# Performance work log

Hardware: AMD Instinct MI355X
Metric: run time of the kernel (lower is better)

Reference implementation:

```python
import jax, jax.numpy as jnp
import numpy as np

NQ = 7
DIM = 2 ** NQ  # 128
N_LAYERS = 3

# Pauli-Z sign tables over the 128 basis states (wire 0 = most significant bit)
_bits = ((np.arange(DIM)[None, :] >> (NQ - 1 - np.arange(NQ)[:, None])) & 1)
_SZ = (1.0 - 2.0 * _bits).astype(np.float32)            # [7, 128]
_SZZ = (_SZ * np.roll(_SZ, -1, axis=0)).astype(np.float32)  # [7, 128], Z_i Z_{(i+1)%7}


def _cnot_perm(c, t):
    # CNOT is a basis-state permutation: flip target bit where control bit = 1
    k = np.arange(DIM)
    return k ^ (((k >> (NQ - 1 - c)) & 1) << (NQ - 1 - t))


def _apply_ry(state, theta, q):
    # state: [B, 128] complex64; theta: [B] or scalar (real)
    B = state.shape[0]
    s = state.reshape(B, 2 ** q, 2, 2 ** (NQ - 1 - q))
    c = jnp.reshape(jnp.cos(0.5 * theta), (-1, 1, 1))
    sn = jnp.reshape(jnp.sin(0.5 * theta), (-1, 1, 1))
    a0, a1 = s[:, :, 0, :], s[:, :, 1, :]
    return jnp.stack([c * a0 - sn * a1, sn * a0 + c * a1], axis=2).reshape(B, DIM)


def _apply_rz(state, theta, q):
    B = state.shape[0]
    s = state.reshape(B, 2 ** q, 2, 2 ** (NQ - 1 - q))
    p = jnp.reshape(jnp.exp(-0.5j * theta), (-1, 1, 1))  # diag(e^{-i t/2}, e^{+i t/2})
    return jnp.stack([p * s[:, :, 0, :], jnp.conj(p) * s[:, :, 1, :]], axis=2).reshape(B, DIM)


def _circuit(x_q, scales, biases, wry, wrz):
    # Batched 7-qubit state-vector simulation of quantum_circuit_v3
    B = x_q.shape[0]
    state = jnp.zeros((B, DIM), jnp.complex64).at[:, 0].set(1.0)
    ang = scales[None, :] * x_q + biases[None, :]  # [B, 7] encoding angles (same every layer)
    for layer in range(N_LAYERS):
        for i in range(NQ):
            state = _apply_ry(state, ang[:, i], i)
        for i in range(NQ):
            state = _apply_ry(state, wry[layer, i], i)
            state = _apply_rz(state, wrz[layer, i], i)
        shift = layer + 1
        for i in range(NQ):
            state = state[:, _cnot_perm(i, (i + shift) % NQ)]
    probs = state.real ** 2 + state.imag ** 2  # [B, 128]
    return jnp.concatenate([probs @ _SZ.T, probs @ _SZZ.T], axis=1)  # [B, 14]


def setup_inputs() -> dict:
    key = jax.random.key(0)
    ks = jax.random.split(key, 16)
    B, F = 32768, 64
    fus_in = 14 + 32 + F  # 110
    lin = lambda k, fi, fo: (0.05 * jax.random.normal(k, (fi, fo), jnp.float32))
    d = {
        "x_q": jax.random.uniform(ks[0], (B, NQ), jnp.float32),
        "x_c": jax.random.normal(ks[1], (B, F), jnp.float32),
        "input_scales": jnp.full((NQ,), np.pi, jnp.float32),
        "input_biases": jnp.zeros((NQ,), jnp.float32),
        "q_params_ry": 0.1 * jax.random.normal(ks[2], (N_LAYERS, NQ), jnp.float32),
        "q_params_rz": 0.1 * jax.random.normal(ks[3], (N_LAYERS, NQ), jnp.float32),
        "enc_w1": lin(ks[4], F, 64), "enc_b1": jnp.zeros((64,), jnp.float32),
        "enc_w2": lin(ks[5], 64, 32), "enc_b2": jnp.zeros((32,), jnp.float32),
        "fus_w1": lin(ks[6], fus_in, 128), "fus_b1": jnp.zeros((128,), jnp.float32),
        "fus_w2": lin(ks[7], 128, 64), "fus_b2": jnp.zeros((64,), jnp.float32),
        "fus_w3": lin(ks[8], 64, 32), "fus_b3": jnp.zeros((32,), jnp.float32),
        "fus_w4": lin(ks[9], 32, 1), "fus_b4": jnp.zeros((1,), jnp.float32),
    }
    return d


def reference(x_q, x_c, input_scales, input_biases, q_params_ry, q_params_rz,
              enc_w1, enc_b1, enc_w2, enc_b2,
              fus_w1, fus_b1, fus_w2, fus_b2, fus_w3, fus_b3, fus_w4, fus_b4):
    q_out = _circuit(x_q, input_scales, input_biases, q_params_ry, q_params_rz)  # [B, 14]
    h = jax.nn.relu(x_c @ enc_w1 + enc_b1)
    c_enc = jax.nn.relu(h @ enc_w2 + enc_b2)  # [B, 32]
    comb = jnp.concatenate([q_out, c_enc, x_c], axis=1)  # [B, 110]
    h = jax.nn.relu(comb @ fus_w1 + fus_b1)
    h = jax.nn.relu(h @ fus_w2 + fus_b2)
    h = jax.nn.relu(h @ fus_w3 + fus_b3)
    return (h @ fus_w4 + fus_b4)[:, 0]  # [B], dropout is identity at inference
```

## Files before the change

kernel.cpp:

```cpp
#include <hip/hip_runtime.h>
#include <math.h>

#define NQ 7
#define DIM 128
#define NLAYERS 3
#define ROWS 64
#define LDS_S 136

typedef __attribute__((ext_vector_type(8))) short bf16x8;
typedef __attribute__((ext_vector_type(4))) float f32x4;
typedef __attribute__((ext_vector_type(4))) unsigned short us4;

__device__ __forceinline__ unsigned short f2bf(float x) {
    union { float f; unsigned int u; } v; v.f = x;
    unsigned int r = v.u + 0x7fff + ((v.u >> 16) & 1);
    return (unsigned short)(r >> 16);
}

constexpr int cperm(int k, int c, int t) {
    return k ^ (((k >> (6 - c)) & 1) << (6 - t));
}
constexpr int lgather(int k, int s) {
    int r = k;
    for (int i = 6; i >= 0; --i) r = cperm(r, i, (i + s) % 7);
    return r;
}

struct Mat { int c[7]; };

constexpr Mat ID{{1, 2, 4, 8, 16, 32, 64}};

constexpr int parity7(int x) { x ^= x >> 4; x ^= x >> 2; x ^= x >> 1; return x & 1; }

constexpr int mapv(const Mat& A, int v) {
    int r = 0;
    for (int j = 0; j < 7; ++j) if ((v >> j) & 1) r ^= A.c[j];
    return r;
}
constexpr Mat matmul(const Mat& A, const Mat& B) {
    Mat m{};
    for (int j = 0; j < 7; ++j) m.c[j] = mapv(A, B.c[j]);
    return m;
}
constexpr Mat matG(int L) {
    Mat m{};
    for (int j = 0; j < 7; ++j) m.c[j] = lgather(1 << j, L + 1);
    return m;
}
constexpr Mat matinv(const Mat& A) {
    int M[7] = {};
    for (int r = 0; r < 7; ++r) {
        int row = 0;
        for (int j = 0; j < 7; ++j) row |= ((A.c[j] >> r) & 1) << j;
        M[r] = row | (1 << (7 + r));
    }
    for (int col = 0; col < 7; ++col) {
        int piv = col;
        while (!((M[piv] >> col) & 1)) ++piv;
        int t = M[col]; M[col] = M[piv]; M[piv] = t;
        for (int r = 0; r < 7; ++r)
            if (r != col && ((M[r] >> col) & 1)) M[r] ^= M[col];
    }
    Mat inv{};
    for (int j = 0; j < 7; ++j) {
        int c = 0;
        for (int r = 0; r < 7; ++r) c |= ((M[r] >> (7 + j)) & 1) << r;
        inv.c[j] = c;
    }
    return inv;
}
constexpr bool isident(const Mat& A) {
    for (int j = 0; j < 7; ++j) if (A.c[j] != (1 << j)) return false;
    return true;
}

constexpr Mat LAM1  = matinv(matG(0));
constexpr Mat LAM2  = matmul(matinv(matG(1)), LAM1);
constexpr Mat LAM3  = matmul(matinv(matG(2)), LAM2);
constexpr Mat LAM1I = matG(0);
constexpr Mat LAM2I = matinv(LAM2);
static_assert(isident(matmul(LAM1, LAM1I)), "lam1 inv");
static_assert(isident(matmul(LAM2, LAM2I)), "lam2 inv");
static_assert(isident(matmul(matG(2), matmul(LAM3, matinv(LAM2)))), "lam3 chain");

constexpr int rowmask(const Mat& A, int b) {
    int r = 0;
    for (int j = 0; j < 7; ++j) r |= ((A.c[j] >> b) & 1) << j;
    return r;
}
constexpr int featM(const Mat& A, int m) {
    int M = 0;
    for (int j = 0; j < 7; ++j) M |= parity7(A.c[j] & m) << j;
    return M;
}
constexpr int szzmask(int i) { return (1 << (6 - i)) | (1 << (6 - ((i + 1) % 7))); }

template<int M>
__device__ __forceinline__ float xsh(float v) {
    if constexpr (M == 1 || M == 2 || M == 3) {
        constexpr int ctrl = (0 ^ M) | ((1 ^ M) << 2) | ((2 ^ M) << 4) | ((3 ^ M) << 6);
        return __int_as_float(__builtin_amdgcn_update_dpp(
            __float_as_int(v), __float_as_int(v), ctrl, 0xF, 0xF, true));
    } else if constexpr (M == 7) {
        return __int_as_float(__builtin_amdgcn_update_dpp(
            __float_as_int(v), __float_as_int(v), 0x141, 0xF, 0xF, true));
    } else if constexpr (M == 15) {
        return __int_as_float(__builtin_amdgcn_update_dpp(
            __float_as_int(v), __float_as_int(v), 0x140, 0xF, 0xF, true));
    } else {
        return __shfl_xor(v, M, 64);
    }
}

template<int D, int R>
__device__ __forceinline__ void ryg(float c, float s, int lane,
                                    float& x0r, float& x0i, float& x1r, float& x1i)
{
    constexpr int  DL = D & 63;
    constexpr int  RL = R & 63;
    constexpr bool D6 = (D >> 6) & 1;
    constexpr bool R6 = (R >> 6) & 1;
    int par = __popc(lane & RL) & 1;
    float ns = -s;
    float sg0 = par ? s : ns;
    float sg1 = R6 ? (par ? ns : s) : sg0;
    float p0r, p0i, p1r, p1i;
    if constexpr (D6) {
        if constexpr (DL == 0) { p0r = x1r; p0i = x1i; p1r = x0r; p1i = x0i; }
        else {
            p0r = xsh<DL>(x1r); p0i = xsh<DL>(x1i);
            p1r = xsh<DL>(x0r); p1i = xsh<DL>(x0i);
        }
    } else {
        p0r = xsh<DL>(x0r); p0i = xsh<DL>(x0i);
        p1r = xsh<DL>(x1r); p1i = xsh<DL>(x1i);
    }
    x0r = fmaf(c, x0r, sg0 * p0r); x0i = fmaf(c, x0i, sg0 * p0i);
    x1r = fmaf(c, x1r, sg1 * p1r); x1i = fmaf(c, x1i, sg1 * p1i);
}

template<int LYR, int I>
__device__ __forceinline__ void rygates(
    const float* trig,
    const float (&dc)[2][NQ], const float (&dsn)[2][NQ], int lane,
    float (&A0r)[2], float (&A0i)[2], float (&A1r)[2], float (&A1i)[2])
{
    if constexpr (I < NQ) {
        constexpr Mat LM  = (LYR == 1) ? LAM1 : LAM2;
        constexpr Mat LMI = (LYR == 1) ? LAM1I : LAM2I;
        constexpr int b   = 6 - I;
        constexpr int D   = mapv(LMI, 1 << b);
        constexpr int R   = rowmask(LM, b);
        float cw = trig[(LYR * NQ + I) * 2 + 0];
        float sw = trig[(LYR * NQ + I) * 2 + 1];
#pragma unroll
        for (int e = 0; e < 2; ++e) {
            float c = dc[e][I] * cw - dsn[e][I] * sw;
            float s = dsn[e][I] * cw + dc[e][I] * sw;
            ryg<D, R>(c, s, lane, A0r[e], A0i[e], A1r[e], A1i[e]);
        }
        rygates<LYR, I + 1>(trig, dc, dsn, lane, A0r, A0i, A1r, A1i);
    }
}

template<int LYR, int Q>
__device__ __forceinline__ void rzrows(const float* __restrict__ wrz, int lane,
                                       float& Aacc, float& Bacc)
{
    if constexpr (Q < NQ) {
        constexpr Mat LM = (LYR == 0) ? ID : ((LYR == 1) ? LAM1 : LAM2);
        constexpr int R  = rowmask(LM, 6 - Q);
        float h = 0.5f * wrz[LYR * NQ + Q];
        float t = (__popc(lane & (R & 63)) & 1) ? -h : h;
        if constexpr ((R >> 6) & 1) Bacc += t; else Aacc += t;
        rzrows<LYR, Q + 1>(wrz, lane, Aacc, Bacc);
    }
}

template<int LYR>
__device__ __forceinline__ void rzlayer(const float* __restrict__ wrz, int lane,
    float (&A0r)[2], float (&A0i)[2], float (&A1r)[2], float (&A1i)[2])
{
    float Aacc = 0.0f, Bacc = 0.0f;
    rzrows<LYR, 0>(wrz, lane, Aacc, Bacc);
    float th0 = Aacc + Bacc, th1 = Aacc - Bacc;
    float c0 = __cosf(th0), s0 = __sinf(th0);
    float c1 = __cosf(th1), s1 = __sinf(th1);
#pragma unroll
    for (int e = 0; e < 2; ++e) {
        float r = A0r[e], im = A0i[e];
        A0r[e] = fmaf(c0, r, s0 * im);
        A0i[e] = fmaf(c0, im, -s0 * r);
        r = A1r[e]; im = A1i[e];
        A1r[e] = fmaf(c1, r, s1 * im);
        A1i[e] = fmaf(c1, im, -s1 * r);
    }
}

template<int M>
__device__ __forceinline__ void bfly(int lane, float& tp, float& tm) {
    float pp = xsh<M>(tp), pm = xsh<M>(tm);
    bool hi = (lane & M) != 0;
    tp = hi ? (pp - tp) : (tp + pp);
    tm = hi ? (pm - tm) : (tm + pm);
}

template<int F>
__device__ __forceinline__ void feats(int lane, float tp, float tm,
                                      float* __restrict__ qo) {
    if constexpr (F < 14) {
        constexpr int m = (F < 7) ? (64 >> F) : szzmask(F - 7);
        constexpr int M = featM(LAM3, m);
        if (lane == (M & 63)) qo[F] = ((M >> 6) & 1) ? tm : tp;
        feats<F + 1>(lane, tp, tm, qo);
    }
}

__global__ __launch_bounds__(256) void circuit_kernel(
    const float* __restrict__ x_q, const float* __restrict__ scales,
    const float* __restrict__ biases,
    const float* __restrict__ wry, const float* __restrict__ wrz,
    const float* __restrict__ ew1, const float* __restrict__ ew2,
    const float* __restrict__ w1,  const float* __restrict__ w2,
    const float* __restrict__ w3,  const float* __restrict__ w4,
    float* __restrict__ q_out,
    unsigned short* __restrict__ ew1t, unsigned short* __restrict__ ew2t,
    unsigned short* __restrict__ w1t,  unsigned short* __restrict__ w2t,
    unsigned short* __restrict__ w3t,  unsigned short* __restrict__ w4t,
    int B)
{
    __shared__ float strig[NLAYERS * NQ * 2];
    const int tid  = threadIdx.x;
    const int lane = tid & 63;

    if (tid < NLAYERS * NQ) {
        float hy = 0.5f * wry[tid];
        strig[tid * 2 + 0] = __cosf(hy);
        strig[tid * 2 + 1] = __sinf(hy);
    }

    if (blockIdx.x < 64) {
        const int gbase  = blockIdx.x * 256 + tid;
        const int stride = 64 * 256;
        for (int i = gbase; i < 16384; i += stride) {
            int n = i >> 7, kp = i & 127;
            unsigned short v = 0;
            if (kp < 64)        v = f2bf(w1[(46 + kp) * 128 + n]);
            else if (kp < 78)   v = f2bf(w1[(kp - 64) * 128 + n]);
            else if (kp < 110)  v = f2bf(w1[(kp - 78 + 14) * 128 + n]);
            w1t[i] = v;
        }
        for (int i = gbase; i < 8192; i += stride) {
            int n = i >> 7, k = i & 127;
            w2t[i] = f2bf(w2[k * 64 + n]);
        }
        for (int i = gbase; i < 4096; i += stride) {
            int n = i >> 6, k = i & 63;
            ew1t[i] = f2bf(ew1[k * 64 + n]);
        }
        for (int i = gbase; i < 2048; i += stride) {
            int n = i >> 6, k = i & 63;
            ew2t[i] = f2bf(ew2[k * 32 + n]);
        }
        for (int i = gbase; i < 2048; i += stride) {
            int n = i >> 6, k = i & 63;
            w3t[i] = f2bf(w3[k * 32 + n]);
        }
        for (int i = gbase; i < 512; i += stride) {
            int n = i >> 5, k = i & 31;
            w4t[i] = (n == 0) ? f2bf(w4[k]) : (unsigned short)0;
        }
    }
    __syncthreads();

    int gtid = blockIdx.x * blockDim.x + tid;
    int wv   = gtid >> 6;
    int e0   = wv * 2;
    if (e0 >= B) return;

    float dc[2][NQ], dsn[2][NQ];
#pragma unroll
    for (int e = 0; e < 2; ++e)
#pragma unroll
        for (int i = 0; i < NQ; ++i) {
            float h = 0.5f * fmaf(scales[i], x_q[(e0 + e) * NQ + i], biases[i]);
            dc[e][i]  = __cosf(h);
            dsn[e][i] = __sinf(h);
        }

    float A0r[2], A0i[2], A1r[2], A1i[2];
#pragma unroll
    for (int e = 0; e < 2; ++e) {
        float cl[NQ], sl[NQ];
#pragma unroll
        for (int i = 0; i < NQ; ++i) {
            float cw = strig[i * 2 + 0], sw = strig[i * 2 + 1];
            cl[i] = dc[e][i] * cw - dsn[e][i] * sw;
            sl[i] = dsn[e][i] * cw + dc[e][i] * sw;
        }
        float f1 = (lane & 32) ? sl[1] : cl[1];
        float f2 = (lane & 16) ? sl[2] : cl[2];
        float f3 = (lane &  8) ? sl[3] : cl[3];
        float f4 = (lane &  4) ? sl[4] : cl[4];
        float f5 = (lane &  2) ? sl[5] : cl[5];
        float f6 = (lane &  1) ? sl[6] : cl[6];
        float pr = (f1 * f2) * (f3 * f4) * (f5 * f6);
        A0r[e] = pr * cl[0]; A0i[e] = 0.0f;
        A1r[e] = pr * sl[0]; A1i[e] = 0.0f;
    }

    rzlayer<0>(wrz, lane, A0r, A0i, A1r, A1i);
    rygates<1, 0>(strig, dc, dsn, lane, A0r, A0i, A1r, A1i);
    rzlayer<1>(wrz, lane, A0r, A0i, A1r, A1i);
    rygates<2, 0>(strig, dc, dsn, lane, A0r, A0i, A1r, A1i);
    rzlayer<2>(wrz, lane, A0r, A0i, A1r, A1i);

#pragma unroll
    for (int e = 0; e < 2; ++e) {
        float p0 = A0r[e] * A0r[e] + A0i[e] * A0i[e];
        float p1 = A1r[e] * A1r[e] + A1i[e] * A1i[e];
        float tp = p0 + p1;
        float tm = p0 - p1;

        bfly<1>(lane, tp, tm);
        bfly<2>(lane, tp, tm);
        bfly<4>(lane, tp, tm);
        bfly<8>(lane, tp, tm);
        bfly<16>(lane, tp, tm);
        bfly<32>(lane, tp, tm);

        feats<0>(lane, tp, tm, q_out + (size_t)(e0 + e) * 14);
    }
}

template<int K, int NTILES, bool RELU>
__device__ __forceinline__ void layer_mfma(
    const unsigned short* src, unsigned short* dst,
    const unsigned short* __restrict__ wt, const float* __restrict__ bias,
    int dstcol, int lane, int wv)
{
    constexpr int KB   = K / 32;
    constexpr int NT_W = (NTILES > 4) ? NTILES / 4 : 1;
    constexpr int MT_W = NTILES / NT_W;
    const int ntile0 = (wv * NT_W) % NTILES;
    const int mtile0 = ((wv * NT_W) / NTILES) * MT_W;
    const int lcol = lane & 15;
    const int lrow = lane >> 4;

    bf16x8 bfrag[NT_W][KB];
    float  bb[NT_W];
#pragma unroll
    for (int n = 0; n < NT_W; ++n) {
#pragma unroll
        for (int kb = 0; kb < KB; ++kb)
            bfrag[n][kb] = *(const bf16x8*)&wt[((ntile0 + n) * 16 + lcol) * K + kb * 32 + lrow * 8];
        bb[n] = bias[(ntile0 + n) * 16 + lcol];
    }

#pragma unroll
    for (int m = 0; m < MT_W; ++m) {
        bf16x8 afrag[KB];
#pragma unroll
        for (int kb = 0; kb < KB; ++kb)
            afrag[kb] = *(const bf16x8*)&src[((mtile0 + m) * 16 + lcol) * LDS_S + kb * 32 + lrow * 8];

        f32x4 acc[NT_W];
#pragma unroll
        for (int n = 0; n < NT_W; ++n) acc[n] = (f32x4){bb[n], bb[n], bb[n], bb[n]};
#pragma unroll
        for (int kb = 0; kb < KB; ++kb)
#pragma unroll
            for (int n = 0; n < NT_W; ++n)
                acc[n] = __builtin_amdgcn_mfma_f32_16x16x32_bf16(afrag[kb], bfrag[n][kb], acc[n], 0, 0, 0);

#pragma unroll
        for (int n = 0; n < NT_W; ++n)
#pragma unroll
            for (int r = 0; r < 4; ++r) {
                float v = acc[n][r];
                if (RELU) v = fmaxf(v, 0.0f);
                dst[((mtile0 + m) * 16 + lrow * 4 + r) * LDS_S + dstcol + (ntile0 + n) * 16 + lcol] = f2bf(v);
            }
    }
}

__global__ __launch_bounds__(256, 4) void mlp_kernel(
    const float* __restrict__ q_out, const float* __restrict__ x_c,
    const unsigned short* __restrict__ ew1t, const float* __restrict__ eb1,
    const unsigned short* __restrict__ ew2t, const float* __restrict__ eb2,
    const unsigned short* __restrict__ w1t,  const float* __restrict__ b1,
    const unsigned short* __restrict__ w2t,  const float* __restrict__ b2,
    const unsigned short* __restrict__ w3t,  const float* __restrict__ b3,
    const unsigned short* __restrict__ w4t,  const float* __restrict__ b4,
    float* __restrict__ out, int B)
{
    __shared__ unsigned short BufA[ROWS * LDS_S];
    __shared__ unsigned short BufB[ROWS * LDS_S];

    const int tid  = threadIdx.x;
    const int lane = tid & 63;
    const int wv   = __builtin_amdgcn_readfirstlane(tid >> 6);
    const int base = blockIdx.x * ROWS;

    {
        const float4* xr = (const float4*)(x_c + (size_t)base * 64);
        for (int i = tid; i < 1024; i += 256) {
            int row = i >> 4, fc = i & 15;
            float4 v = xr[i];
            us4 b;
            b.x = f2bf(v.x); b.y = f2bf(v.y); b.z = f2bf(v.z); b.w = f2bf(v.w);
            *(us4*)&BufA[row * LDS_S + fc * 4] = b;
        }
    }
    for (int i = tid; i < 64 * 14; i += 256) {
        int row = i / 14, k = i - row * 14;
        BufA[row * LDS_S + 64 + k] = f2bf(q_out[(size_t)(base + row) * 14 + k]);
    }
    for (int i = tid; i < 64 * 18; i += 256) {
        int row = i / 18, k = i - row * 18;
        BufA[row * LDS_S + 110 + k] = 0;
    }
    __syncthreads();

    layer_mfma<64, 4, true>(BufA, BufB, ew1t, eb1, 0, lane, wv);
    __syncthreads();
    layer_mfma<64, 2, true>(BufB, BufA, ew2t, eb2, 78, lane, wv);
    __syncthreads();
    layer_mfma<128, 8, true>(BufA, BufB, w1t, b1, 0, lane, wv);
    __syncthreads();
    layer_mfma<128, 4, true>(BufB, BufA, w2t, b2, 0, lane, wv);
    __syncthreads();
    layer_mfma<64, 2, true>(BufA, BufB, w3t, b3, 0, lane, wv);
    __syncthreads();

    {
        const int lcol = lane & 15;
        const int lrow = lane >> 4;
        bf16x8 a = *(const bf16x8*)&BufB[(wv * 16 + lcol) * LDS_S + lrow * 8];
        bf16x8 b = *(const bf16x8*)&w4t[lcol * 32 + lrow * 8];
        float bv = b4[0];
        f32x4 acc = (f32x4){bv, bv, bv, bv};
        acc = __builtin_amdgcn_mfma_f32_16x16x32_bf16(a, b, acc, 0, 0, 0);
        if (lcol == 0) {
            float4 o; o.x = acc[0]; o.y = acc[1]; o.z = acc[2]; o.w = acc[3];
            *(float4*)(out + base + wv * 16 + lrow * 4) = o;
        }
    }
}

extern "C" void kernel_launch(void* const* d_in, const int* in_sizes, int n_in,
                              void* d_out, int out_size, void* d_ws, size_t ws_size,
                              hipStream_t stream)
{
    const float* x_q     = (const float*)d_in[0];
    const float* x_c     = (const float*)d_in[1];
    const float* scales  = (const float*)d_in[2];
    const float* biases  = (const float*)d_in[3];
    const float* wry     = (const float*)d_in[4];
    const float* wrz     = (const float*)d_in[5];
    const float* enc_w1  = (const float*)d_in[6];
    const float* enc_b1  = (const float*)d_in[7];
    const float* enc_w2  = (const float*)d_in[8];
    const float* enc_b2  = (const float*)d_in[9];
    const float* fus_w1  = (const float*)d_in[10];
    const float* fus_b1  = (const float*)d_in[11];
    const float* fus_w2  = (const float*)d_in[12];
    const float* fus_b2  = (const float*)d_in[13];
    const float* fus_w3  = (const float*)d_in[14];
    const float* fus_b3  = (const float*)d_in[15];
    const float* fus_w4  = (const float*)d_in[16];
    const float* fus_b4  = (const float*)d_in[17];
    float* out = (float*)d_out;

    int B = in_sizes[0] / NQ;

    float* ws    = (float*)d_ws;
    float* q_out = ws;
    unsigned short* wsh = (unsigned short*)(q_out + (size_t)B * 14);
    unsigned short* w1t  = wsh;
    unsigned short* w2t  = w1t + 16384;
    unsigned short* ew1t = w2t + 8192;
    unsigned short* ew2t = ew1t + 4096;
    unsigned short* w3t  = ew2t + 2048;
    unsigned short* w4t  = w3t + 2048;

    int circ_blocks = ((B / 2) * 64 + 255) / 256;
    circuit_kernel<<<circ_blocks, 256, 0, stream>>>(
        x_q, scales, biases, wry, wrz,
        enc_w1, enc_w2, fus_w1, fus_w2, fus_w3, fus_w4,
        q_out, ew1t, ew2t, w1t, w2t, w3t, w4t, B);

    int row_blocks = B / ROWS;
    mlp_kernel<<<row_blocks, 256, 0, stream>>>(q_out, x_c,
                                               ew1t, enc_b1, ew2t, enc_b2,
                                               w1t, fus_b1, w2t, fus_b2,
                                               w3t, fus_b3, w4t, fus_b4,
                                               out, B);
}
```

Measured before the change: 38.64 us.

## Pack circuit state as float2, swizzle shuffles, per-wave MLP without block syncs

The circuit kernel now holds the two batch elements per wave as float2 vectors, which allows packed FP32 math. Small xor-shuffles now use DPP or ds_swizzle instead of shfl. Feature extraction becomes a single bpermute gather that writes padded 16-float rows, so stores are coalesced. The MLP kernel gives each wave its own 16 rows with private LDS buffers, which removes all __syncthreads, but each wave must now load every weight fragment itself from global or cache.

```diff
diff --git a/kernel.cpp b/kernel.cpp
--- a/kernel.cpp
+++ b/kernel.cpp
@@ -9,12 +9,17 @@
 
 typedef __attribute__((ext_vector_type(8))) short bf16x8;
 typedef __attribute__((ext_vector_type(4))) float f32x4;
+typedef __attribute__((ext_vector_type(2))) float f32x2;
 typedef __attribute__((ext_vector_type(4))) unsigned short us4;
 
 __device__ __forceinline__ unsigned short f2bf(float x) {
     union { float f; unsigned int u; } v; v.f = x;
     unsigned int r = v.u + 0x7fff + ((v.u >> 16) & 1);
     return (unsigned short)(r >> 16);
+}
+__device__ __forceinline__ f32x2 sp(float x) { return (f32x2){x, x}; }
+__device__ __forceinline__ f32x2 sel2(int c, f32x2 a, f32x2 b) {
+    f32x2 r; r.x = c ? a.x : b.x; r.y = c ? a.y : b.y; return r;
 }
 
 constexpr int cperm(int k, int c, int t) {
@@ -94,6 +99,16 @@
     return M;
 }
 constexpr int szzmask(int i) { return (1 << (6 - i)) | (1 << (6 - ((i + 1) % 7))); }
+constexpr int kmask(int k) { return (k < 7) ? (64 >> k) : szzmask(k - 7); }
+constexpr unsigned pack_feat(int base) {
+    unsigned r = 0;
+    for (int j = 0; j < 4; ++j) {
+        int k = base + j;
+        unsigned e = (k < 14) ? (unsigned)featM(LAM3, kmask(k)) : 0u;
+        r |= e << (8 * j);
+    }
+    return r;
+}
 
 template<int M>
 __device__ __forceinline__ float xsh(float v) {
@@ -104,46 +119,59 @@
     } else if constexpr (M == 7) {
         return __int_as_float(__builtin_amdgcn_update_dpp(
             __float_as_int(v), __float_as_int(v), 0x141, 0xF, 0xF, true));
+    } else if constexpr (M == 8) {
+        return __int_as_float(__builtin_amdgcn_update_dpp(
+            __float_as_int(v), __float_as_int(v), 0x128, 0xF, 0xF, true));
     } else if constexpr (M == 15) {
         return __int_as_float(__builtin_amdgcn_update_dpp(
             __float_as_int(v), __float_as_int(v), 0x140, 0xF, 0xF, true));
+    } else if constexpr (M < 32) {
+        return __int_as_float(__builtin_amdgcn_ds_swizzle(
+            __float_as_int(v), (M << 10) | 0x1F));
     } else {
         return __shfl_xor(v, M, 64);
     }
 }
+template<int M>
+__device__ __forceinline__ f32x2 xsh2(f32x2 v) {
+    f32x2 r; r.x = xsh<M>(v.x); r.y = xsh<M>(v.y); return r;
+}
+
+__device__ __forceinline__ float bpermf(int addr, float v) {
+    return __int_as_float(__builtin_amdgcn_ds_bpermute(addr, __float_as_int(v)));
+}
 
 template<int D, int R>
-__device__ __forceinline__ void ryg(float c, float s, int lane,
-                                    float& x0r, float& x0i, float& x1r, float& x1i)
+__device__ __forceinline__ void ryg(f32x2 c, f32x2 s, int lane,
+                                    f32x2& x0r, f32x2& x0i, f32x2& x1r, f32x2& x1i)
 {
     constexpr int  DL = D & 63;
     constexpr int  RL = R & 63;
     constexpr bool D6 = (D >> 6) & 1;
     constexpr bool R6 = (R >> 6) & 1;
     int par = __popc(lane & RL) & 1;
-    float ns = -s;
-    float sg0 = par ? s : ns;
-    float sg1 = R6 ? (par ? ns : s) : sg0;
-    float p0r, p0i, p1r, p1i;
+    f32x2 ns  = -s;
+    f32x2 sg0 = sel2(par, s, ns);
+    f32x2 sg1 = R6 ? sel2(par, ns, s) : sg0;
+    f32x2 p0r, p0i, p1r, p1i;
     if constexpr (D6) {
         if constexpr (DL == 0) { p0r = x1r; p0i = x1i; p1r = x0r; p1i = x0i; }
         else {
-            p0r = xsh<DL>(x1r); p0i = xsh<DL>(x1i);
-            p1r = xsh<DL>(x0r); p1i = xsh<DL>(x0i);
+            p0r = xsh2<DL>(x1r); p0i = xsh2<DL>(x1i);
+            p1r = xsh2<DL>(x0r); p1i = xsh2<DL>(x0i);
         }
     } else {
-        p0r = xsh<DL>(x0r); p0i = xsh<DL>(x0i);
-        p1r = xsh<DL>(x1r); p1i = xsh<DL>(x1i);
-    }
-    x0r = fmaf(c, x0r, sg0 * p0r); x0i = fmaf(c, x0i, sg0 * p0i);
-    x1r = fmaf(c, x1r, sg1 * p1r); x1i = fmaf(c, x1i, sg1 * p1i);
+        p0r = xsh2<DL>(x0r); p0i = xsh2<DL>(x0i);
+        p1r = xsh2<DL>(x1r); p1i = xsh2<DL>(x1i);
+    }
+    x0r = c * x0r + sg0 * p0r;  x0i = c * x0i + sg0 * p0i;
+    x1r = c * x1r + sg1 * p1r;  x1i = c * x1i + sg1 * p1i;
 }
 
 template<int LYR, int I>
 __device__ __forceinline__ void rygates(
-    const float* trig,
-    const float (&dc)[2][NQ], const float (&dsn)[2][NQ], int lane,
-    float (&A0r)[2], float (&A0i)[2], float (&A1r)[2], float (&A1i)[2])
+    const float* trig, const f32x2 (&dc)[NQ], const f32x2 (&dsn)[NQ], int lane,
+    f32x2& A0r, f32x2& A0i, f32x2& A1r, f32x2& A1i)
 {
     if constexpr (I < NQ) {
         constexpr Mat LM  = (LYR == 1) ? LAM1 : LAM2;
@@ -153,12 +181,9 @@
         constexpr int R   = rowmask(LM, b);
         float cw = trig[(LYR * NQ + I) * 2 + 0];
         float sw = trig[(LYR * NQ + I) * 2 + 1];
-#pragma unroll
-        for (int e = 0; e < 2; ++e) {
-            float c = dc[e][I] * cw - dsn[e][I] * sw;
-            float s = dsn[e][I] * cw + dc[e][I] * sw;
-            ryg<D, R>(c, s, lane, A0r[e], A0i[e], A1r[e], A1i[e]);
-        }
+        f32x2 c = dc[I] * sp(cw) - dsn[I] * sp(sw);
+        f32x2 s = dsn[I] * sp(cw) + dc[I] * sp(sw);
+        ryg<D, R>(c, s, lane, A0r, A0i, A1r, A1i);
         rygates<LYR, I + 1>(trig, dc, dsn, lane, A0r, A0i, A1r, A1i);
     }
 }
@@ -179,41 +204,28 @@
 
 template<int LYR>
 __device__ __forceinline__ void rzlayer(const float* __restrict__ wrz, int lane,
-    float (&A0r)[2], float (&A0i)[2], float (&A1r)[2], float (&A1i)[2])
+    f32x2& A0r, f32x2& A0i, f32x2& A1r, f32x2& A1i)
 {
     float Aacc = 0.0f, Bacc = 0.0f;
     rzrows<LYR, 0>(wrz, lane, Aacc, Bacc);
     float th0 = Aacc + Bacc, th1 = Aacc - Bacc;
     float c0 = __cosf(th0), s0 = __sinf(th0);
     float c1 = __cosf(th1), s1 = __sinf(th1);
-#pragma unroll
-    for (int e = 0; e < 2; ++e) {
-        float r = A0r[e], im = A0i[e];
-        A0r[e] = fmaf(c0, r, s0 * im);
-        A0i[e] = fmaf(c0, im, -s0 * r);
-        r = A1r[e]; im = A1i[e];
-        A1r[e] = fmaf(c1, r, s1 * im);
-        A1i[e] = fmaf(c1, im, -s1 * r);
-    }
+    f32x2 r, im;
+    r = A0r; im = A0i;
+    A0r = sp(c0) * r  + sp(s0) * im;
+    A0i = sp(c0) * im - sp(s0) * r;
+    r = A1r; im = A1i;
+    A1r = sp(c1) * r  + sp(s1) * im;
+    A1i = sp(c1) * im - sp(s1) * r;
 }
 
 template<int M>
-__device__ __forceinline__ void bfly(int lane, float& tp, float& tm) {
-    float pp = xsh<M>(tp), pm = xsh<M>(tm);
-    bool hi = (lane & M) != 0;
-    tp = hi ? (pp - tp) : (tp + pp);
-    tm = hi ? (pm - tm) : (tm + pm);
-}
-
-template<int F>
-__device__ __forceinline__ void feats(int lane, float tp, float tm,
-                                      float* __restrict__ qo) {
-    if constexpr (F < 14) {
-        constexpr int m = (F < 7) ? (64 >> F) : szzmask(F - 7);
-        constexpr int M = featM(LAM3, m);
-        if (lane == (M & 63)) qo[F] = ((M >> 6) & 1) ? tm : tp;
-        feats<F + 1>(lane, tp, tm, qo);
-    }
+__device__ __forceinline__ void bfly2(int lane, f32x2& tp, f32x2& tm) {
+    f32x2 pp = xsh2<M>(tp), pm = xsh2<M>(tm);
+    int hi = lane & M;
+    tp = sel2(hi, pp - tp, tp + pp);
+    tm = sel2(hi, pm - tm, tm + pm);
 }
 
 __global__ __launch_bounds__(256) void circuit_kernel(
@@ -278,35 +290,33 @@
     int e0   = wv * 2;
     if (e0 >= B) return;
 
-    float dc[2][NQ], dsn[2][NQ];
-#pragma unroll
-    for (int e = 0; e < 2; ++e)
-#pragma unroll
-        for (int i = 0; i < NQ; ++i) {
-            float h = 0.5f * fmaf(scales[i], x_q[(e0 + e) * NQ + i], biases[i]);
-            dc[e][i]  = __cosf(h);
-            dsn[e][i] = __sinf(h);
-        }
-
-    float A0r[2], A0i[2], A1r[2], A1i[2];
-#pragma unroll
-    for (int e = 0; e < 2; ++e) {
-        float cl[NQ], sl[NQ];
+    f32x2 dc[NQ], dsn[NQ];
+#pragma unroll
+    for (int i = 0; i < NQ; ++i) {
+        float h0 = 0.5f * fmaf(scales[i], x_q[(size_t)e0 * NQ + i], biases[i]);
+        float h1 = 0.5f * fmaf(scales[i], x_q[(size_t)(e0 + 1) * NQ + i], biases[i]);
+        dc[i]  = (f32x2){__cosf(h0), __cosf(h1)};
+        dsn[i] = (f32x2){__sinf(h0), __sinf(h1)};
+    }
+
+    f32x2 A0r, A0i = sp(0.0f), A1r, A1i = sp(0.0f);
+    {
+        f32x2 cl[NQ], sl[NQ];
 #pragma unroll
         for (int i = 0; i < NQ; ++i) {
             float cw = strig[i * 2 + 0], sw = strig[i * 2 + 1];
-            cl[i] = dc[e][i] * cw - dsn[e][i] * sw;
-            sl[i] = dsn[e][i] * cw + dc[e][i] * sw;
-        }
-        float f1 = (lane & 32) ? sl[1] : cl[1];
-        float f2 = (lane & 16) ? sl[2] : cl[2];
-        float f3 = (lane &  8) ? sl[3] : cl[3];
-        float f4 = (lane &  4) ? sl[4] : cl[4];
-        float f5 = (lane &  2) ? sl[5] : cl[5];
-        float f6 = (lane &  1) ? sl[6] : cl[6];
-        float pr = (f1 * f2) * (f3 * f4) * (f5 * f6);
-        A0r[e] = pr * cl[0]; A0i[e] = 0.0f;
-        A1r[e] = pr * sl[0]; A1i[e] = 0.0f;
+            cl[i] = dc[i] * sp(cw) - dsn[i] * sp(sw);
+            sl[i] = dsn[i] * sp(cw) + dc[i] * sp(sw);
+        }
+        f32x2 f1 = sel2(lane & 32, sl[1], cl[1]);
+        f32x2 f2 = sel2(lane & 16, sl[2], cl[2]);
+        f32x2 f3 = sel2(lane &  8, sl[3], cl[3]);
+        f32x2 f4 = sel2(lane &  4, sl[4], cl[4]);
+        f32x2 f5 = sel2(lane &  2, sl[5], cl[5]);
+        f32x2 f6 = sel2(lane &  1, sl[6], cl[6]);
+        f32x2 pr = (f1 * f2) * (f3 * f4) * (f5 * f6);
+        A0r = pr * cl[0];
+        A1r = pr * sl[0];
     }
 
     rzlayer<0>(wrz, lane, A0r, A0i, A1r, A1i);
@@ -315,76 +325,72 @@
     rygates<2, 0>(strig, dc, dsn, lane, A0r, A0i, A1r, A1i);
     rzlayer<2>(wrz, lane, A0r, A0i, A1r, A1i);
 
-#pragma unroll
-    for (int e = 0; e < 2; ++e) {
-        float p0 = A0r[e] * A0r[e] + A0i[e] * A0i[e];
-        float p1 = A1r[e] * A1r[e] + A1i[e] * A1i[e];
-        float tp = p0 + p1;
-        float tm = p0 - p1;
-
-        bfly<1>(lane, tp, tm);
-        bfly<2>(lane, tp, tm);
-        bfly<4>(lane, tp, tm);
-        bfly<8>(lane, tp, tm);
-        bfly<16>(lane, tp, tm);
-        bfly<32>(lane, tp, tm);
-
-        feats<0>(lane, tp, tm, q_out + (size_t)(e0 + e) * 14);
-    }
-}
-
-template<int K, int NTILES, bool RELU>
-__device__ __forceinline__ void layer_mfma(
+    f32x2 p0 = A0r * A0r + A0i * A0i;
+    f32x2 p1 = A1r * A1r + A1i * A1i;
+    f32x2 tp = p0 + p1;
+    f32x2 tm = p0 - p1;
+
+    bfly2<1>(lane, tp, tm);
+    bfly2<2>(lane, tp, tm);
+    bfly2<4>(lane, tp, tm);
+    bfly2<8>(lane, tp, tm);
+    bfly2<16>(lane, tp, tm);
+    bfly2<32>(lane, tp, tm);
+
+    {
+        constexpr unsigned P0 = pack_feat(0),  P1 = pack_feat(4);
+        constexpr unsigned P2 = pack_feat(8),  P3 = pack_feat(12);
+        int k = lane & 15;
+        unsigned wlo  = (k & 4) ? P1 : P0;
+        unsigned whi  = (k & 4) ? P3 : P2;
+        unsigned word = (k & 8) ? whi : wlo;
+        unsigned entry = (word >> ((k & 3) * 8)) & 127u;
+        int addr   = (int)(entry & 63u) << 2;
+        int useTm  = (int)(entry & 64u);
+        int e      = (lane >> 4) & 1;
+        float vpx = bpermf(addr, tp.x), vpy = bpermf(addr, tp.y);
+        float vmx = bpermf(addr, tm.x), vmy = bpermf(addr, tm.y);
+        float vp = e ? vpy : vpx;
+        float vm = e ? vmy : vmx;
+        float val = useTm ? vm : vp;
+        if (lane < 32) q_out[(size_t)e0 * 16 + lane] = val;
+    }
+}
+
+template<int K, int NT, bool RELU>
+__device__ __forceinline__ void wlayer(
     const unsigned short* src, unsigned short* dst,
     const unsigned short* __restrict__ wt, const float* __restrict__ bias,
-    int dstcol, int lane, int wv)
-{
-    constexpr int KB   = K / 32;
-    constexpr int NT_W = (NTILES > 4) ? NTILES / 4 : 1;
-    constexpr int MT_W = NTILES / NT_W;
-    const int ntile0 = (wv * NT_W) % NTILES;
-    const int mtile0 = ((wv * NT_W) / NTILES) * MT_W;
+    int dstcol, int lane)
+{
+    constexpr int KB = K / 32;
     const int lcol = lane & 15;
     const int lrow = lane >> 4;
 
-    bf16x8 bfrag[NT_W][KB];
-    float  bb[NT_W];
-#pragma unroll
-    for (int n = 0; n < NT_W; ++n) {
-#pragma unroll
-        for (int kb = 0; kb < KB; ++kb)
-            bfrag[n][kb] = *(const bf16x8*)&wt[((ntile0 + n) * 16 + lcol) * K + kb * 32 + lrow * 8];
-        bb[n] = bias[(ntile0 + n) * 16 + lcol];
-    }
-
-#pragma unroll
-    for (int m = 0; m < MT_W; ++m) {
-        bf16x8 afrag[KB];
-#pragma unroll
-        for (int kb = 0; kb < KB; ++kb)
-            afrag[kb] = *(const bf16x8*)&src[((mtile0 + m) * 16 + lcol) * LDS_S + kb * 32 + lrow * 8];
-
-        f32x4 acc[NT_W];
-#pragma unroll
-        for (int n = 0; n < NT_W; ++n) acc[n] = (f32x4){bb[n], bb[n], bb[n], bb[n]};
-#pragma unroll
-        for (int kb = 0; kb < KB; ++kb)
-#pragma unroll
-            for (int n = 0; n < NT_W; ++n)
-                acc[n] = __builtin_amdgcn_mfma_f32_16x16x32_bf16(afrag[kb], bfrag[n][kb], acc[n], 0, 0, 0);
-
-#pragma unroll
-        for (int n = 0; n < NT_W; ++n)
-#pragma unroll
-            for (int r = 0; r < 4; ++r) {
-                float v = acc[n][r];
-                if (RELU) v = fmaxf(v, 0.0f);
-                dst[((mtile0 + m) * 16 + lrow * 4 + r) * LDS_S + dstcol + (ntile0 + n) * 16 + lcol] = f2bf(v);
-            }
-    }
-}
-
-__global__ __launch_bounds__(256, 4) void mlp_kernel(
+    bf16x8 a[KB];
+#pragma unroll
+    for (int kb = 0; kb < KB; ++kb)
+        a[kb] = *(const bf16x8*)&src[lcol * LDS_S + kb * 32 + lrow * 8];
+
+#pragma unroll
+    for (int n = 0; n < NT; ++n) {
+        float bb = bias[n * 16 + lcol];
+        f32x4 acc = (f32x4){bb, bb, bb, bb};
+#pragma unroll
+        for (int kb = 0; kb < KB; ++kb) {
+            bf16x8 b = *(const bf16x8*)&wt[(n * 16 + lcol) * K + kb * 32 + lrow * 8];
+            acc = __builtin_amdgcn_mfma_f32_16x16x32_bf16(a[kb], b, acc, 0, 0, 0);
+        }
+#pragma unroll
+        for (int r = 0; r < 4; ++r) {
+            float v = acc[r];
+            if (RELU) v = fmaxf(v, 0.0f);
+            dst[(lrow * 4 + r) * LDS_S + dstcol + n * 16 + lcol] = f2bf(v);
+        }
+    }
+}
+
+__global__ __launch_bounds__(256) void mlp_kernel(
     const float* __restrict__ q_out, const float* __restrict__ x_c,
     const unsigned short* __restrict__ ew1t, const float* __restrict__ eb1,
     const unsigned short* __restrict__ ew2t, const float* __restrict__ eb2,
@@ -394,56 +400,58 @@
     const unsigned short* __restrict__ w4t,  const float* __restrict__ b4,
     float* __restrict__ out, int B)
 {
-    __shared__ unsigned short BufA[ROWS * LDS_S];
-    __shared__ unsigned short BufB[ROWS * LDS_S];
-
-    const int tid  = threadIdx.x;
-    const int lane = tid & 63;
-    const int wv   = __builtin_amdgcn_readfirstlane(tid >> 6);
-    const int base = blockIdx.x * ROWS;
+    __shared__ unsigned short Buf[4 * 2 * 16 * LDS_S];
+
+    const int tid   = threadIdx.x;
+    const int lane  = tid & 63;
+    const int wv    = tid >> 6;
+    const int rbase = blockIdx.x * ROWS + wv * 16;
+
+    unsigned short* bufA = Buf + wv * (2 * 16 * LDS_S);
+    unsigned short* bufB = bufA + 16 * LDS_S;
 
     {
-        const float4* xr = (const float4*)(x_c + (size_t)base * 64);
-        for (int i = tid; i < 1024; i += 256) {
-            int row = i >> 4, fc = i & 15;
-            float4 v = xr[i];
+        const int srow = lane >> 2;
+#pragma unroll
+        for (int it = 0; it < 4; ++it) {
+            int fc = (lane & 3) + it * 4;
+            float4 v = *(const float4*)&x_c[(size_t)(rbase + srow) * 64 + fc * 4];
             us4 b;
             b.x = f2bf(v.x); b.y = f2bf(v.y); b.z = f2bf(v.z); b.w = f2bf(v.w);
-            *(us4*)&BufA[row * LDS_S + fc * 4] = b;
-        }
-    }
-    for (int i = tid; i < 64 * 14; i += 256) {
-        int row = i / 14, k = i - row * 14;
-        BufA[row * LDS_S + 64 + k] = f2bf(q_out[(size_t)(base + row) * 14 + k]);
-    }
-    for (int i = tid; i < 64 * 18; i += 256) {
-        int row = i / 18, k = i - row * 18;
-        BufA[row * LDS_S + 110 + k] = 0;
-    }
-    __syncthreads();
-
-    layer_mfma<64, 4, true>(BufA, BufB, ew1t, eb1, 0, lane, wv);
-    __syncthreads();
-    layer_mfma<64, 2, true>(BufB, BufA, ew2t, eb2, 78, lane, wv);
-    __syncthreads();
-    layer_mfma<128, 8, true>(BufA, BufB, w1t, b1, 0, lane, wv);
-    __syncthreads();
-    layer_mfma<128, 4, true>(BufB, BufA, w2t, b2, 0, lane, wv);
-    __syncthreads();
-    layer_mfma<64, 2, true>(BufA, BufB, w3t, b3, 0, lane, wv);
-    __syncthreads();
+            *(us4*)&bufA[srow * LDS_S + fc * 4] = b;
+        }
+    }
+#pragma unroll
+    for (int it = 0; it < 4; ++it) {
+        int idx = lane + it * 64;
+        int row = idx >> 4, k = idx & 15;
+        bufA[row * LDS_S + 64 + k] = f2bf(q_out[(size_t)(rbase + row) * 16 + k]);
+    }
+#pragma unroll
+    for (int it = 0; it < 2; ++it) {
+        int idx = lane + it * 64;
+        int row = idx >> 3, j = idx & 7;
+        *(unsigned int*)&bufA[row * LDS_S + 112 + 2 * j] = 0;
+    }
+    if (lane < 16) *(unsigned int*)&bufA[lane * LDS_S + 110] = 0;
+
+    wlayer< 64, 4, true>(bufA, bufB, ew1t, eb1,  0, lane);
+    wlayer< 64, 2, true>(bufB, bufA, ew2t, eb2, 78, lane);
+    wlayer<128, 8, true>(bufA, bufB, w1t,  b1,   0, lane);
+    wlayer<128, 4, true>(bufB, bufA, w2t,  b2,   0, lane);
+    wlayer< 64, 2, true>(bufA, bufB, w3t,  b3,   0, lane);
 
     {
         const int lcol = lane & 15;
         const int lrow = lane >> 4;
-        bf16x8 a = *(const bf16x8*)&BufB[(wv * 16 + lcol) * LDS_S + lrow * 8];
+        bf16x8 a = *(const bf16x8*)&bufB[lcol * LDS_S + lrow * 8];
         bf16x8 b = *(const bf16x8*)&w4t[lcol * 32 + lrow * 8];
         float bv = b4[0];
         f32x4 acc = (f32x4){bv, bv, bv, bv};
         acc = __builtin_amdgcn_mfma_f32_16x16x32_bf16(a, b, acc, 0, 0, 0);
         if (lcol == 0) {
             float4 o; o.x = acc[0]; o.y = acc[1]; o.z = acc[2]; o.w = acc[3];
-            *(float4*)(out + base + wv * 16 + lrow * 4) = o;
+            *(float4*)(out + rbase + lrow * 4) = o;
         }
     }
 }
@@ -476,7 +484,7 @@
 
     float* ws    = (float*)d_ws;
     float* q_out = ws;
-    unsigned short* wsh = (unsigned short*)(q_out + (size_t)B * 14);
+    unsigned short* wsh = (unsigned short*)(q_out + (size_t)B * 16);
     unsigned short* w1t  = wsh;
     unsigned short* w2t  = w1t + 16384;
     unsigned short* ew1t = w2t + 8192;
```

Measured after the change: 41.93 us. 1.09x slower.
